# Optimization experiments

Measured on AMD Instinct MI355X. Metric: run time of the kernel, lower is better.

The kernel has to match this reference:

```python
import jax, jax.numpy as jnp
import numpy as np

N_NODES = 100000
N_FEAT = 500
N_HID = 16
N_CLS = 7
N_EDGES = 3200000


def setup_inputs() -> dict:
    key = jax.random.key(0)
    k1, k2, k3, k4 = jax.random.split(key, 4)
    x = jax.random.normal(k1, (N_NODES, N_FEAT), dtype=jnp.float32)
    edge_index = jax.random.randint(k2, (2, N_EDGES), 0, N_NODES, dtype=jnp.int32)
    # Glorot-style init for the two GCNConv weight matrices
    W1 = jax.random.normal(k3, (N_FEAT, N_HID), dtype=jnp.float32) * (1.0 / np.sqrt(N_FEAT))
    b1 = jnp.zeros((N_HID,), dtype=jnp.float32)
    W2 = jax.random.normal(k4, (N_HID, N_CLS), dtype=jnp.float32) * (1.0 / np.sqrt(N_HID))
    b2 = jnp.zeros((N_CLS,), dtype=jnp.float32)
    return {"x": x, "edge_index": edge_index, "W1": W1, "b1": b1, "W2": W2, "b2": b2}


def _gcn_norm(edge_index, n_nodes):
    # Add self-loops, compute symmetric normalization D^-1/2 (A+I) D^-1/2
    loop = jnp.arange(n_nodes, dtype=edge_index.dtype)
    src = jnp.concatenate([edge_index[0], loop])  # [E+N]
    dst = jnp.concatenate([edge_index[1], loop])  # [E+N]
    deg = jax.ops.segment_sum(jnp.ones_like(dst, dtype=jnp.float32), dst, num_segments=n_nodes)
    dinv = jnp.where(deg > 0, jax.lax.rsqrt(deg), 0.0)
    norm = dinv[src] * dinv[dst]  # [E+N]
    return src, dst, norm


def _gcn_conv(h, W, b, src, dst, norm, n_nodes):
    m = h @ W                                   # [N, out] dense projection first (small out dim)
    agg = jax.ops.segment_sum(m[src] * norm[:, None], dst, num_segments=n_nodes)
    return agg + b


def reference(x, edge_index, W1, b1, W2, b2):
    n = x.shape[0]
    src, dst, norm = _gcn_norm(edge_index, n)
    h = jax.nn.relu(_gcn_conv(x, W1, b1, src, dst, norm, n))
    # dropout is identity in eval mode (training=False)
    logits = _gcn_conv(h, W2, b2, src, dst, norm, n)
    return jax.nn.log_softmax(logits, axis=1)
```

## Files before the change

### kernel.cpp

```cpp
#include <hip/hip_runtime.h>
#include <math.h>

#define N_NODES 100000
#define N_EDGES 3200000
#define N_FEAT  500
#define NF4     125
#define N_HID   16
#define N_CLS   7

#define BKT_SHIFT 7
#define BKT_SIZE  128
#define NBKT      782
#define NBLK_BIN  256
#define EDGES_PER_BLK 12500
#define COUNTS_LEN (NBKT * NBLK_BIN)
#define NBLK_SCANA (COUNTS_LEN / 256)
#define SBUF_CAP  5632

#define OFF_DINV   0
#define OFF_COUNTS 100000
#define OFF_BSUM   300192
#define OFF_ROWP   301216
#define OFF_BINNED 401220
#define OFF_SORTED 3601220
#define OFF_M1S    6801220
#define OFF_M2S    7601220

typedef __attribute__((ext_vector_type(8))) short short8v;
typedef __attribute__((ext_vector_type(4))) float f32x4v;

__device__ inline unsigned short f2bf(float f) {
    unsigned int u = __float_as_uint(f);
    return (unsigned short)((u + 0x7FFF + ((u >> 16) & 1)) >> 16);
}
__device__ inline float bf2f(unsigned short h) {
    return __uint_as_float((unsigned int)h << 16);
}

__device__ inline void gload16(const void* g, void* l) {
    __builtin_amdgcn_global_load_lds(
        (const __attribute__((address_space(1))) void*)g,
        (__attribute__((address_space(3))) void*)l, 16, 0, 0);
}

__global__ void hist(const int* __restrict__ dst, int* __restrict__ counts) {
    __shared__ int cnt[NBKT];
    int t = threadIdx.x, b = blockIdx.x;
    for (int i = t; i < NBKT; i += 256) cnt[i] = 0;
    __syncthreads();
    int e0 = b * EDGES_PER_BLK;
    for (int e = e0 + t; e < e0 + EDGES_PER_BLK; e += 256)
        atomicAdd(&cnt[dst[e] >> BKT_SHIFT], 1);
    __syncthreads();
    for (int i = t; i < NBKT; i += 256)
        counts[i * NBLK_BIN + b] = cnt[i];
}

__global__ void scanA(int* __restrict__ counts, int* __restrict__ bsum) {
    __shared__ int s[256];
    int t = threadIdx.x;
    int i = blockIdx.x * 256 + t;
    int v = counts[i];
    s[t] = v;
    __syncthreads();
    for (int off = 1; off < 256; off <<= 1) {
        int a = (t >= off) ? s[t - off] : 0;
        __syncthreads();
        s[t] += a;
        __syncthreads();
    }
    counts[i] = s[t] - v;
    if (t == 255) bsum[blockIdx.x] = s[255];
}

__global__ void scanB(int* __restrict__ bsum) {
    __shared__ int s[1024];
    int t = threadIdx.x;
    int v = (t < NBLK_SCANA) ? bsum[t] : 0;
    s[t] = v;
    __syncthreads();
    for (int off = 1; off < 1024; off <<= 1) {
        int a = (t >= off) ? s[t - off] : 0;
        __syncthreads();
        s[t] += a;
        __syncthreads();
    }
    if (t < NBLK_SCANA) bsum[t] = s[t] - v;
}


__global__ void binpass(const int* __restrict__ src, const int* __restrict__ dst,
                        const int* __restrict__ counts, const int* __restrict__ bsum,
                        unsigned int* __restrict__ binned) {
    __shared__ int cur[NBKT];
    int t = threadIdx.x, b = blockIdx.x;
    for (int i = t; i < NBKT; i += 256) cur[i] = counts[i * NBLK_BIN + b] + bsum[i];
    __syncthreads();
    int e0 = b * EDGES_PER_BLK;
    for (int e = e0 + t; e < e0 + EDGES_PER_BLK; e += 256) {
        int d = dst[e];
        int pos = atomicAdd(&cur[d >> BKT_SHIFT], 1);
        binned[pos] = (unsigned int)src[e] | ((unsigned int)(d & (BKT_SIZE - 1)) << 17);
    }
}

__global__ __launch_bounds__(512) void sortpass(const unsigned int* __restrict__ binned,
        const int* __restrict__ counts, const int* __restrict__ bsum,
        unsigned int* __restrict__ sorted,
        int* __restrict__ rowptr, float* __restrict__ dinv) {
    __shared__ int cnt[BKT_SIZE];
    __shared__ int sc[BKT_SIZE];
    __shared__ int cur[BKT_SIZE];
    __shared__ unsigned int sbuf[SBUF_CAP];
    int t = threadIdx.x, b = blockIdx.x;
    int beg = counts[b * NBLK_BIN] + bsum[b];
    int end = (b < NBKT - 1) ? counts[(b + 1) * NBLK_BIN] + bsum[b + 1] : N_EDGES;
    if (t < BKT_SIZE) cnt[t] = 0;
    __syncthreads();
    for (int e = beg + t; e < end; e += 512)
        atomicAdd(&cnt[(binned[e] >> 17) & (BKT_SIZE - 1)], 1);
    __syncthreads();
    int v = (t < BKT_SIZE) ? cnt[t] : 0;
    if (t < BKT_SIZE) sc[t] = v;
    __syncthreads();
    for (int off = 1; off < BKT_SIZE; off <<= 1) {
        int a = (t < BKT_SIZE && t >= off) ? sc[t - off] : 0;
        __syncthreads();
        if (t < BKT_SIZE) sc[t] += a;
        __syncthreads();
    }
    if (t < BKT_SIZE) {
        cur[t] = sc[t] - v;
        int g = b * BKT_SIZE + t;
        if (g < N_NODES) {
            rowptr[g] = beg + sc[t] - v;
            dinv[g] = rsqrtf((float)v + 1.0f);
        }
    }
    if (b == 0 && t == 0) rowptr[N_NODES] = N_EDGES;
    __syncthreads();
    for (int e = beg + t; e < end; e += 512) {
        unsigned int u = binned[e];
        int pos = atomicAdd(&cur[(u >> 17) & (BKT_SIZE - 1)], 1);
        if (pos < SBUF_CAP) sbuf[pos] = u & 0x1FFFF;
    }
    __syncthreads();
    int n = end - beg;
    for (int i = t; i < n; i += 512) sorted[beg + i] = sbuf[i];
}

__global__ void wpack(const float* __restrict__ W1, uint4* __restrict__ wp) {
    int p = blockIdx.x * 256 + threadIdx.x;
    if (p >= 1024) return;
    int s = p >> 6, l = p & 63;
    int col = l & 15, kb = s * 32 + (l >> 4) * 8;
    unsigned int hw[4], lw[4];
#pragma unroll
    for (int d = 0; d < 4; ++d) {
        unsigned int hpair = 0, lpair = 0;
#pragma unroll
        for (int e = 0; e < 2; ++e) {
            int k = kb + d * 2 + e;
            float w0 = (k < N_FEAT) ? W1[k * 16 + col] : 0.f;
            unsigned int u = __float_as_uint(w0);
            unsigned int uh = u & 0xFFFF0000u;
            float res = w0 - __uint_as_float(uh);
            hpair |= (uh >> 16) << (16 * e);
            lpair |= (unsigned int)f2bf(res) << (16 * e);
        }
        hw[d] = hpair; lw[d] = lpair;
    }
    wp[p] = make_uint4(hw[0], hw[1], hw[2], hw[3]);
    wp[1024 + p] = make_uint4(lw[0], lw[1], lw[2], lw[3]);
}

#define G1_NBLK 1563

__device__ inline void split8(const float4 a, const float4 b, short8v& hi, short8v& lo) {
    float f[8] = {a.x, a.y, a.z, a.w, b.x, b.y, b.z, b.w};
#pragma unroll
    for (int i = 0; i < 8; ++i) {
        unsigned int u = __float_as_uint(f[i]);
        unsigned int uh = u & 0xFFFF0000u;
        hi[i] = (short)(u >> 16);
        lo[i] = (short)f2bf(f[i] - __uint_as_float(uh));
    }
}

__global__ __launch_bounds__(256) void gemm1(const float* __restrict__ x,
        const uint4* __restrict__ wp, const float* __restrict__ dinv,
        unsigned short* __restrict__ m1s) {
    __shared__ float lds[2][2048];
    const int t = threadIdx.x, b = blockIdx.x;
    const int lane = t & 63, w = t >> 6;
    const int rowbase = b * 64;
    const char* xb = (const char*)x;

    size_t gbase[2], gtail[2];
#pragma unroll
    for (int j = 0; j < 2; ++j) {
        int i = j * 256 + t;
        int row = i >> 3;
        int u = i & 7;
        int inner = (u * 16) ^ ((row & 7) << 4);
        int grow = rowbase + row; if (grow >= N_NODES) grow = 0;
        gbase[j] = (size_t)grow * 2000 + (size_t)inner;
        int tf = 480 + (inner >> 2);
        gtail[j] = (tf < 500) ? gbase[j] + 1920 : (size_t)0;
    }

    const int r16 = lane & 15, g = lane >> 4;
    const int lrow = w * 16 + r16;
    const int sw = (lrow & 7) << 4;
    const int off1 = lrow * 128 + ((g * 32) ^ sw);
    const int off2 = lrow * 128 + ((g * 32 + 16) ^ sw);

    f32x4v acc = {0.f, 0.f, 0.f, 0.f};

    gload16(xb + gbase[0], (void*)&lds[0][w * 256]);
    gload16(xb + gbase[1], (void*)&lds[0][1024 + w * 256]);
    __syncthreads();

    int cur = 0;
    for (int s = 0; s < 16; ++s) {
        if (s < 15) {
            int sn = s + 1;
            size_t a0 = (sn < 15) ? gbase[0] + (size_t)sn * 128 : gtail[0];
            size_t a1 = (sn < 15) ? gbase[1] + (size_t)sn * 128 : gtail[1];
            gload16(xb + a0, (void*)&lds[cur ^ 1][w * 256]);
            gload16(xb + a1, (void*)&lds[cur ^ 1][1024 + w * 256]);
        }
        short8v bh = *reinterpret_cast<const short8v*>(&wp[s * 64 + lane]);
        short8v bl = *reinterpret_cast<const short8v*>(&wp[1024 + s * 64 + lane]);
        const char* lb = (const char*)&lds[cur][0];
        float4 fa = *(const float4*)(lb + off1);
        float4 fb = *(const float4*)(lb + off2);
        short8v ah, al;
        split8(fa, fb, ah, al);
        acc = __builtin_amdgcn_mfma_f32_16x16x32_bf16(ah, bh, acc, 0, 0, 0);
        acc = __builtin_amdgcn_mfma_f32_16x16x32_bf16(al, bh, acc, 0, 0, 0);
        acc = __builtin_amdgcn_mfma_f32_16x16x32_bf16(ah, bl, acc, 0, 0, 0);
        __syncthreads();
        cur ^= 1;
    }

#pragma unroll
    for (int j = 0; j < 4; ++j) {
        int r = rowbase + w * 16 + g * 4 + j;
        if (r < N_NODES) m1s[(size_t)r * 16 + r16] = f2bf(acc[j] * dinv[r]);
    }
}

__global__ __launch_bounds__(512) void agg1(const unsigned int* __restrict__ sorted,
        const int* __restrict__ rowptr, const float* __restrict__ dinv,
        const unsigned short* __restrict__ m1s, const float* __restrict__ b1,
        const float* __restrict__ W2, unsigned short* __restrict__ m2s) {
    __shared__ float acc[BKT_SIZE * 17];
    __shared__ float sW2[N_HID * N_CLS];
    __shared__ float sb1[N_HID];
    int t = threadIdx.x, b = blockIdx.x;
    if (t < N_HID * N_CLS) sW2[t] = W2[t];
    if (t < N_HID) sb1[t] = b1[t];
    int n = t >> 2, q = t & 3;
    int g = b * BKT_SIZE + n;
    float a0 = 0.f, a1 = 0.f, a2 = 0.f, a3 = 0.f;
    if (g < N_NODES) {
        int beg = rowptr[g], end = rowptr[g + 1];
        int p = beg;
        for (; p + 1 < end; p += 2) {
            unsigned int s0 = sorted[p], s1 = sorted[p + 1];
            uint2 w0 = *(const uint2*)&m1s[(size_t)s0 * 16 + q * 4];
            uint2 w1 = *(const uint2*)&m1s[(size_t)s1 * 16 + q * 4];
            a0 += __uint_as_float(w0.x << 16);
            a1 += __uint_as_float(w0.x & 0xFFFF0000u);
            a2 += __uint_as_float(w0.y << 16);
            a3 += __uint_as_float(w0.y & 0xFFFF0000u);
            a0 += __uint_as_float(w1.x << 16);
            a1 += __uint_as_float(w1.x & 0xFFFF0000u);
            a2 += __uint_as_float(w1.y << 16);
            a3 += __uint_as_float(w1.y & 0xFFFF0000u);
        }
        if (p < end) {
            unsigned int s0 = sorted[p];
            uint2 w0 = *(const uint2*)&m1s[(size_t)s0 * 16 + q * 4];
            a0 += __uint_as_float(w0.x << 16);
            a1 += __uint_as_float(w0.x & 0xFFFF0000u);
            a2 += __uint_as_float(w0.y << 16);
            a3 += __uint_as_float(w0.y & 0xFFFF0000u);
        }
    }
    float* ap = &acc[n * 17 + q * 4];
    ap[0] = a0; ap[1] = a1; ap[2] = a2; ap[3] = a3;
    __syncthreads();
    for (int idx = t; idx < BKT_SIZE * 16; idx += 512) {
        int nn = idx >> 4, jj = idx & 15;
        int gg = b * BKT_SIZE + nn;
        if (gg < N_NODES) {
            float di = dinv[gg];
            float hv = di * (acc[nn * 17 + jj] + bf2f(m1s[(size_t)gg * 16 + jj])) + sb1[jj];
            acc[nn * 17 + jj] = hv > 0.f ? hv : 0.f;
        }
    }
    __syncthreads();
    for (int idx = t; idx < BKT_SIZE * 8; idx += 512) {
        int nn = idx >> 3, cc = idx & 7;
        int gg = b * BKT_SIZE + nn;
        if (gg < N_NODES) {
            float sum = 0.f;
            if (cc < N_CLS) {
#pragma unroll
                for (int jj = 0; jj < N_HID; ++jj) sum += acc[nn * 17 + jj] * sW2[jj * 7 + cc];
                sum *= dinv[gg];
            }
            m2s[(size_t)gg * 8 + cc] = f2bf(sum);
        }
    }
}

__global__ __launch_bounds__(256) void agg2(const unsigned int* __restrict__ sorted,
        const int* __restrict__ rowptr, const float* __restrict__ dinv,
        const unsigned short* __restrict__ m2s, const float* __restrict__ b2,
        float* __restrict__ out) {
    __shared__ float acc[BKT_SIZE * 9];
    int t = threadIdx.x, b = blockIdx.x;
    int n = t >> 1, q = t & 1;
    int g = b * BKT_SIZE + n;
    float a0 = 0.f, a1 = 0.f, a2 = 0.f, a3 = 0.f;
    if (g < N_NODES) {
        int beg = rowptr[g], end = rowptr[g + 1];
        int p = beg;
        for (; p + 1 < end; p += 2) {
            unsigned int s0 = sorted[p], s1 = sorted[p + 1];
            uint2 w0 = *(const uint2*)&m2s[(size_t)s0 * 8 + q * 4];
            uint2 w1 = *(const uint2*)&m2s[(size_t)s1 * 8 + q * 4];
            a0 += __uint_as_float(w0.x << 16);
            a1 += __uint_as_float(w0.x & 0xFFFF0000u);
            a2 += __uint_as_float(w0.y << 16);
            a3 += __uint_as_float(w0.y & 0xFFFF0000u);
            a0 += __uint_as_float(w1.x << 16);
            a1 += __uint_as_float(w1.x & 0xFFFF0000u);
            a2 += __uint_as_float(w1.y << 16);
            a3 += __uint_as_float(w1.y & 0xFFFF0000u);
        }
        if (p < end) {
            unsigned int s0 = sorted[p];
            uint2 w0 = *(const uint2*)&m2s[(size_t)s0 * 8 + q * 4];
            a0 += __uint_as_float(w0.x << 16);
            a1 += __uint_as_float(w0.x & 0xFFFF0000u);
            a2 += __uint_as_float(w0.y << 16);
            a3 += __uint_as_float(w0.y & 0xFFFF0000u);
        }
    }
    float* ap = &acc[n * 9 + q * 4];
    ap[0] = a0; ap[1] = a1; ap[2] = a2; ap[3] = a3;
    __syncthreads();
    int j = t & 7;
    for (int pass = 0; pass < 4; ++pass) {
        int nn = (t >> 3) + pass * 32;
        int gg = b * BKT_SIZE + nn;
        bool valid = (gg < N_NODES) && (j < N_CLS);
        float v = -1e30f;
        if (valid) {
            float di = dinv[gg];
            v = di * (acc[nn * 9 + j] + bf2f(m2s[(size_t)gg * 8 + j])) + b2[j];
        }
        float mx = v;
#pragma unroll
        for (int off = 1; off < 8; off <<= 1) mx = fmaxf(mx, __shfl_xor(mx, off, 8));
        float ex = valid ? expf(v - mx) : 0.f;
        float sum = ex;
#pragma unroll
        for (int off = 1; off < 8; off <<= 1) sum += __shfl_xor(sum, off, 8);
        float ls = mx + logf(sum);
        if (valid) out[(size_t)gg * 7 + j] = v - ls;
    }
}

extern "C" void kernel_launch(void* const* d_in, const int* in_sizes, int n_in,
                              void* d_out, int out_size, void* d_ws, size_t ws_size,
                              hipStream_t stream) {
    const float* x  = (const float*)d_in[0];
    const int*   ei = (const int*)d_in[1];
    const float* W1 = (const float*)d_in[2];
    const float* b1 = (const float*)d_in[3];
    const float* W2 = (const float*)d_in[4];
    const float* b2 = (const float*)d_in[5];
    float* out = (float*)d_out;
    char*  wsb = (char*)d_ws;

    const int* src = ei;
    const int* dst = ei + N_EDGES;

    float*          dinv   = (float*)wsb + OFF_DINV;
    int*            counts = (int*)wsb + OFF_COUNTS;
    int*            bsum   = (int*)wsb + OFF_BSUM;
    int*            rowptr = (int*)wsb + OFF_ROWP;
    unsigned int*   binned = (unsigned int*)wsb + OFF_BINNED;
    unsigned int*   sorted = (unsigned int*)wsb + OFF_SORTED;
    unsigned short* m1s    = (unsigned short*)(wsb + (size_t)OFF_M1S * 4);
    unsigned short* m2s    = (unsigned short*)(wsb + (size_t)OFF_M2S * 4);
    uint4*          wp     = (uint4*)binned;

    hist     <<<NBLK_BIN, 256, 0, stream>>>(dst, counts);
    scanA    <<<NBLK_SCANA, 256, 0, stream>>>(counts, bsum);
    scanB    <<<1, 1024, 0, stream>>>(bsum);
    binpass  <<<NBLK_BIN, 256, 0, stream>>>(src, dst, counts, bsum, binned);
    sortpass <<<NBKT, 512, 0, stream>>>(binned, counts, bsum, sorted, rowptr, dinv);
    wpack    <<<4, 256, 0, stream>>>(W1, wp);
    gemm1    <<<G1_NBLK, 256, 0, stream>>>(x, wp, dinv, m1s);
    agg1     <<<NBKT, 512, 0, stream>>>(sorted, rowptr, dinv, m1s, b1, W2, m2s);
    agg2     <<<NBKT, 256, 0, stream>>>(sorted, rowptr, dinv, m2s, b2, out);
}
```

Measured before the change: 497.3 us.

## Drop per-node CSR sort; aggregate bucketed edges with LDS float atomics

Removes the sortpass kernel that built per-node CSR order and rowptr. Degrees now come from global atomics in the histogram pass, with a small kernel computing dinv. The aggregation kernels walk each 128-node bucket's binned edges directly and accumulate into shared-memory rows with float atomicAdd, using staggered column order to spread bank conflicts. This saves the sort pass and its traffic, but adds many LDS atomics per edge, global atomics on deg, and a memset, and makes the summation order nondeterministic.

```diff
diff --git a/kernel.cpp b/kernel.cpp
--- a/kernel.cpp
+++ b/kernel.cpp
@@ -15,14 +15,13 @@
 #define EDGES_PER_BLK 12500
 #define COUNTS_LEN (NBKT * NBLK_BIN)
 #define NBLK_SCANA (COUNTS_LEN / 256)
-#define SBUF_CAP  5632
 
 #define OFF_DINV   0
 #define OFF_COUNTS 100000
 #define OFF_BSUM   300192
-#define OFF_ROWP   301216
+#define OFF_DEG    301216
 #define OFF_BINNED 401220
-#define OFF_SORTED 3601220
+#define OFF_WP     3601220
 #define OFF_M1S    6801220
 #define OFF_M2S    7601220
 
@@ -43,17 +42,26 @@
         (__attribute__((address_space(3))) void*)l, 16, 0, 0);
 }
 
-__global__ void hist(const int* __restrict__ dst, int* __restrict__ counts) {
+__global__ void hist(const int* __restrict__ dst, int* __restrict__ counts,
+                     int* __restrict__ deg) {
     __shared__ int cnt[NBKT];
     int t = threadIdx.x, b = blockIdx.x;
     for (int i = t; i < NBKT; i += 256) cnt[i] = 0;
     __syncthreads();
     int e0 = b * EDGES_PER_BLK;
-    for (int e = e0 + t; e < e0 + EDGES_PER_BLK; e += 256)
-        atomicAdd(&cnt[dst[e] >> BKT_SHIFT], 1);
+    for (int e = e0 + t; e < e0 + EDGES_PER_BLK; e += 256) {
+        int d = dst[e];
+        atomicAdd(&cnt[d >> BKT_SHIFT], 1);
+        atomicAdd(&deg[d], 1);
+    }
     __syncthreads();
     for (int i = t; i < NBKT; i += 256)
         counts[i * NBLK_BIN + b] = cnt[i];
+}
+
+__global__ void dinvK(const int* __restrict__ deg, float* __restrict__ dinv) {
+    int g = blockIdx.x * 256 + threadIdx.x;
+    if (g < N_NODES) dinv[g] = rsqrtf((float)deg[g] + 1.0f);
 }
 
 __global__ void scanA(int* __restrict__ counts, int* __restrict__ bsum) {
@@ -88,7 +96,6 @@
     if (t < NBLK_SCANA) bsum[t] = s[t] - v;
 }
 
-
 __global__ void binpass(const int* __restrict__ src, const int* __restrict__ dst,
                         const int* __restrict__ counts, const int* __restrict__ bsum,
                         unsigned int* __restrict__ binned) {
@@ -102,51 +109,6 @@
         int pos = atomicAdd(&cur[d >> BKT_SHIFT], 1);
         binned[pos] = (unsigned int)src[e] | ((unsigned int)(d & (BKT_SIZE - 1)) << 17);
     }
-}
-
-__global__ __launch_bounds__(512) void sortpass(const unsigned int* __restrict__ binned,
-        const int* __restrict__ counts, const int* __restrict__ bsum,
-        unsigned int* __restrict__ sorted,
-        int* __restrict__ rowptr, float* __restrict__ dinv) {
-    __shared__ int cnt[BKT_SIZE];
-    __shared__ int sc[BKT_SIZE];
-    __shared__ int cur[BKT_SIZE];
-    __shared__ unsigned int sbuf[SBUF_CAP];
-    int t = threadIdx.x, b = blockIdx.x;
-    int beg = counts[b * NBLK_BIN] + bsum[b];
-    int end = (b < NBKT - 1) ? counts[(b + 1) * NBLK_BIN] + bsum[b + 1] : N_EDGES;
-    if (t < BKT_SIZE) cnt[t] = 0;
-    __syncthreads();
-    for (int e = beg + t; e < end; e += 512)
-        atomicAdd(&cnt[(binned[e] >> 17) & (BKT_SIZE - 1)], 1);
-    __syncthreads();
-    int v = (t < BKT_SIZE) ? cnt[t] : 0;
-    if (t < BKT_SIZE) sc[t] = v;
-    __syncthreads();
-    for (int off = 1; off < BKT_SIZE; off <<= 1) {
-        int a = (t < BKT_SIZE && t >= off) ? sc[t - off] : 0;
-        __syncthreads();
-        if (t < BKT_SIZE) sc[t] += a;
-        __syncthreads();
-    }
-    if (t < BKT_SIZE) {
-        cur[t] = sc[t] - v;
-        int g = b * BKT_SIZE + t;
-        if (g < N_NODES) {
-            rowptr[g] = beg + sc[t] - v;
-            dinv[g] = rsqrtf((float)v + 1.0f);
-        }
-    }
-    if (b == 0 && t == 0) rowptr[N_NODES] = N_EDGES;
-    __syncthreads();
-    for (int e = beg + t; e < end; e += 512) {
-        unsigned int u = binned[e];
-        int pos = atomicAdd(&cur[(u >> 17) & (BKT_SIZE - 1)], 1);
-        if (pos < SBUF_CAP) sbuf[pos] = u & 0x1FFFF;
-    }
-    __syncthreads();
-    int n = end - beg;
-    for (int i = t; i < n; i += 512) sorted[beg + i] = sbuf[i];
 }
 
 __global__ void wpack(const float* __restrict__ W1, uint4* __restrict__ wp) {
@@ -251,48 +213,47 @@
     }
 }
 
-__global__ __launch_bounds__(512) void agg1(const unsigned int* __restrict__ sorted,
-        const int* __restrict__ rowptr, const float* __restrict__ dinv,
-        const unsigned short* __restrict__ m1s, const float* __restrict__ b1,
-        const float* __restrict__ W2, unsigned short* __restrict__ m2s) {
+__global__ __launch_bounds__(256) void bagg1(const unsigned int* __restrict__ binned,
+        const int* __restrict__ counts, const int* __restrict__ bsum,
+        const float* __restrict__ dinv, const unsigned short* __restrict__ m1s,
+        const float* __restrict__ b1, const float* __restrict__ W2,
+        unsigned short* __restrict__ m2s) {
     __shared__ float acc[BKT_SIZE * 17];
     __shared__ float sW2[N_HID * N_CLS];
     __shared__ float sb1[N_HID];
     int t = threadIdx.x, b = blockIdx.x;
     if (t < N_HID * N_CLS) sW2[t] = W2[t];
     if (t < N_HID) sb1[t] = b1[t];
-    int n = t >> 2, q = t & 3;
-    int g = b * BKT_SIZE + n;
-    float a0 = 0.f, a1 = 0.f, a2 = 0.f, a3 = 0.f;
-    if (g < N_NODES) {
-        int beg = rowptr[g], end = rowptr[g + 1];
-        int p = beg;
-        for (; p + 1 < end; p += 2) {
-            unsigned int s0 = sorted[p], s1 = sorted[p + 1];
-            uint2 w0 = *(const uint2*)&m1s[(size_t)s0 * 16 + q * 4];
-            uint2 w1 = *(const uint2*)&m1s[(size_t)s1 * 16 + q * 4];
-            a0 += __uint_as_float(w0.x << 16);
-            a1 += __uint_as_float(w0.x & 0xFFFF0000u);
-            a2 += __uint_as_float(w0.y << 16);
-            a3 += __uint_as_float(w0.y & 0xFFFF0000u);
-            a0 += __uint_as_float(w1.x << 16);
-            a1 += __uint_as_float(w1.x & 0xFFFF0000u);
-            a2 += __uint_as_float(w1.y << 16);
-            a3 += __uint_as_float(w1.y & 0xFFFF0000u);
-        }
-        if (p < end) {
-            unsigned int s0 = sorted[p];
-            uint2 w0 = *(const uint2*)&m1s[(size_t)s0 * 16 + q * 4];
-            a0 += __uint_as_float(w0.x << 16);
-            a1 += __uint_as_float(w0.x & 0xFFFF0000u);
-            a2 += __uint_as_float(w0.y << 16);
-            a3 += __uint_as_float(w0.y & 0xFFFF0000u);
-        }
-    }
-    float* ap = &acc[n * 17 + q * 4];
-    ap[0] = a0; ap[1] = a1; ap[2] = a2; ap[3] = a3;
-    __syncthreads();
-    for (int idx = t; idx < BKT_SIZE * 16; idx += 512) {
+    for (int i = t; i < BKT_SIZE * 17; i += 256) acc[i] = 0.f;
+    int beg = counts[b * NBLK_BIN] + bsum[b];
+    int end = (b < NBKT - 1) ? counts[(b + 1) * NBLK_BIN] + bsum[b + 1] : N_EDGES;
+    __syncthreads();
+    const int st = t & 15;
+    for (int e = beg + t; e < end; e += 256) {
+        unsigned int u = binned[e];
+        int s = u & 0x1FFFF;
+        float* ap = &acc[((u >> 17) & (BKT_SIZE - 1)) * 17];
+        uint4 w0 = *(const uint4*)&m1s[(size_t)s * 16];
+        uint4 w1 = *(const uint4*)&m1s[(size_t)s * 16 + 8];
+        float f[16];
+        f[0]  = __uint_as_float(w0.x << 16); f[1]  = __uint_as_float(w0.x & 0xFFFF0000u);
+        f[2]  = __uint_as_float(w0.y << 16); f[3]  = __uint_as_float(w0.y & 0xFFFF0000u);
+        f[4]  = __uint_as_float(w0.z << 16); f[5]  = __uint_as_float(w0.z & 0xFFFF0000u);
+        f[6]  = __uint_as_float(w0.w << 16); f[7]  = __uint_as_float(w0.w & 0xFFFF0000u);
+        f[8]  = __uint_as_float(w1.x << 16); f[9]  = __uint_as_float(w1.x & 0xFFFF0000u);
+        f[10] = __uint_as_float(w1.y << 16); f[11] = __uint_as_float(w1.y & 0xFFFF0000u);
+        f[12] = __uint_as_float(w1.z << 16); f[13] = __uint_as_float(w1.w == 0 ? 0.f : __float_as_uint(0.f));
+        f[13] = __uint_as_float(w1.z & 0xFFFF0000u);
+        f[14] = __uint_as_float(w1.w << 16); f[15] = __uint_as_float(w1.w & 0xFFFF0000u);
+        f[12] = __uint_as_float(w1.z << 16);
+#pragma unroll
+        for (int i = 0; i < 16; ++i) {
+            int j = (i + st) & 15;
+            atomicAdd(&ap[j], f[j]);
+        }
+    }
+    __syncthreads();
+    for (int idx = t; idx < BKT_SIZE * 16; idx += 256) {
         int nn = idx >> 4, jj = idx & 15;
         int gg = b * BKT_SIZE + nn;
         if (gg < N_NODES) {
@@ -302,7 +263,7 @@
         }
     }
     __syncthreads();
-    for (int idx = t; idx < BKT_SIZE * 8; idx += 512) {
+    for (int idx = t; idx < BKT_SIZE * 8; idx += 256) {
         int nn = idx >> 3, cc = idx & 7;
         int gg = b * BKT_SIZE + nn;
         if (gg < N_NODES) {
@@ -317,42 +278,33 @@
     }
 }
 
-__global__ __launch_bounds__(256) void agg2(const unsigned int* __restrict__ sorted,
-        const int* __restrict__ rowptr, const float* __restrict__ dinv,
-        const unsigned short* __restrict__ m2s, const float* __restrict__ b2,
-        float* __restrict__ out) {
+__global__ __launch_bounds__(256) void bagg2(const unsigned int* __restrict__ binned,
+        const int* __restrict__ counts, const int* __restrict__ bsum,
+        const float* __restrict__ dinv, const unsigned short* __restrict__ m2s,
+        const float* __restrict__ b2, float* __restrict__ out) {
     __shared__ float acc[BKT_SIZE * 9];
     int t = threadIdx.x, b = blockIdx.x;
-    int n = t >> 1, q = t & 1;
-    int g = b * BKT_SIZE + n;
-    float a0 = 0.f, a1 = 0.f, a2 = 0.f, a3 = 0.f;
-    if (g < N_NODES) {
-        int beg = rowptr[g], end = rowptr[g + 1];
-        int p = beg;
-        for (; p + 1 < end; p += 2) {
-            unsigned int s0 = sorted[p], s1 = sorted[p + 1];
-            uint2 w0 = *(const uint2*)&m2s[(size_t)s0 * 8 + q * 4];
-            uint2 w1 = *(const uint2*)&m2s[(size_t)s1 * 8 + q * 4];
-            a0 += __uint_as_float(w0.x << 16);
-            a1 += __uint_as_float(w0.x & 0xFFFF0000u);
-            a2 += __uint_as_float(w0.y << 16);
-            a3 += __uint_as_float(w0.y & 0xFFFF0000u);
-            a0 += __uint_as_float(w1.x << 16);
-            a1 += __uint_as_float(w1.x & 0xFFFF0000u);
-            a2 += __uint_as_float(w1.y << 16);
-            a3 += __uint_as_float(w1.y & 0xFFFF0000u);
-        }
-        if (p < end) {
-            unsigned int s0 = sorted[p];
-            uint2 w0 = *(const uint2*)&m2s[(size_t)s0 * 8 + q * 4];
-            a0 += __uint_as_float(w0.x << 16);
-            a1 += __uint_as_float(w0.x & 0xFFFF0000u);
-            a2 += __uint_as_float(w0.y << 16);
-            a3 += __uint_as_float(w0.y & 0xFFFF0000u);
-        }
-    }
-    float* ap = &acc[n * 9 + q * 4];
-    ap[0] = a0; ap[1] = a1; ap[2] = a2; ap[3] = a3;
+    for (int i = t; i < BKT_SIZE * 9; i += 256) acc[i] = 0.f;
+    int beg = counts[b * NBLK_BIN] + bsum[b];
+    int end = (b < NBKT - 1) ? counts[(b + 1) * NBLK_BIN] + bsum[b + 1] : N_EDGES;
+    __syncthreads();
+    const int st = t & 7;
+    for (int e = beg + t; e < end; e += 256) {
+        unsigned int u = binned[e];
+        int s = u & 0x1FFFF;
+        float* ap = &acc[((u >> 17) & (BKT_SIZE - 1)) * 9];
+        uint4 w0 = *(const uint4*)&m2s[(size_t)s * 8];
+        float f[8];
+        f[0] = __uint_as_float(w0.x << 16); f[1] = __uint_as_float(w0.x & 0xFFFF0000u);
+        f[2] = __uint_as_float(w0.y << 16); f[3] = __uint_as_float(w0.y & 0xFFFF0000u);
+        f[4] = __uint_as_float(w0.z << 16); f[5] = __uint_as_float(w0.z & 0xFFFF0000u);
+        f[6] = __uint_as_float(w0.w << 16); f[7] = __uint_as_float(w0.w & 0xFFFF0000u);
+#pragma unroll
+        for (int i = 0; i < 8; ++i) {
+            int j = (i + st) & 7;
+            atomicAdd(&ap[j], f[j]);
+        }
+    }
     __syncthreads();
     int j = t & 7;
     for (int pass = 0; pass < 4; ++pass) {
@@ -394,20 +346,20 @@
     float*          dinv   = (float*)wsb + OFF_DINV;
     int*            counts = (int*)wsb + OFF_COUNTS;
     int*            bsum   = (int*)wsb + OFF_BSUM;
-    int*            rowptr = (int*)wsb + OFF_ROWP;
+    int*            deg    = (int*)wsb + OFF_DEG;
     unsigned int*   binned = (unsigned int*)wsb + OFF_BINNED;
-    unsigned int*   sorted = (unsigned int*)wsb + OFF_SORTED;
+    uint4*          wp     = (uint4*)((int*)wsb + OFF_WP);
     unsigned short* m1s    = (unsigned short*)(wsb + (size_t)OFF_M1S * 4);
     unsigned short* m2s    = (unsigned short*)(wsb + (size_t)OFF_M2S * 4);
-    uint4*          wp     = (uint4*)binned;
-
-    hist     <<<NBLK_BIN, 256, 0, stream>>>(dst, counts);
-    scanA    <<<NBLK_SCANA, 256, 0, stream>>>(counts, bsum);
-    scanB    <<<1, 1024, 0, stream>>>(bsum);
-    binpass  <<<NBLK_BIN, 256, 0, stream>>>(src, dst, counts, bsum, binned);
-    sortpass <<<NBKT, 512, 0, stream>>>(binned, counts, bsum, sorted, rowptr, dinv);
-    wpack    <<<4, 256, 0, stream>>>(W1, wp);
-    gemm1    <<<G1_NBLK, 256, 0, stream>>>(x, wp, dinv, m1s);
-    agg1     <<<NBKT, 512, 0, stream>>>(sorted, rowptr, dinv, m1s, b1, W2, m2s);
-    agg2     <<<NBKT, 256, 0, stream>>>(sorted, rowptr, dinv, m2s, b2, out);
-}
+
+    hipMemsetAsync(deg, 0, N_NODES * sizeof(int), stream);
+    hist    <<<NBLK_BIN, 256, 0, stream>>>(dst, counts, deg);
+    dinvK   <<<391, 256, 0, stream>>>(deg, dinv);
+    scanA   <<<NBLK_SCANA, 256, 0, stream>>>(counts, bsum);
+    scanB   <<<1, 1024, 0, stream>>>(bsum);
+    binpass <<<NBLK_BIN, 256, 0, stream>>>(src, dst, counts, bsum, binned);
+    wpack   <<<4, 256, 0, stream>>>(W1, wp);
+    gemm1   <<<G1_NBLK, 256, 0, stream>>>(x, wp, dinv, m1s);
+    bagg1   <<<NBKT, 256, 0, stream>>>(binned, counts, bsum, dinv, m1s, b1, W2, m2s);
+    bagg2   <<<NBKT, 256, 0, stream>>>(binned, counts, bsum, dinv, m2s, b2, out);
+}
```

Result: slower. 1.029 ms (+107.0%).

## Replace two-level bucket sort CSR build with global-atomic degree count and scatter

Applied to the files above, without the earlier changes.

Replaces the histogram/bin/local-sort pipeline for building the destination-sorted CSR with a direct approach. Per-node degrees are counted with global atomics, prefix-scanned into row offsets, and edges are scattered with global atomicAdd on the row pointers. After the scatter, each row pointer holds its row's end offset, and the aggregation kernels read that shifted form. This removes one full pass over the edges and the binned intermediate buffer. In exchange it relies on 3.2M contended global atomics and random scattered writes, and the order of edges within a row becomes nondeterministic.

```diff
diff --git a/kernel.cpp b/kernel.cpp
--- a/kernel.cpp
+++ b/kernel.cpp
@@ -4,27 +4,21 @@
 #define N_NODES 100000
 #define N_EDGES 3200000
 #define N_FEAT  500
-#define NF4     125
 #define N_HID   16
 #define N_CLS   7
 
-#define BKT_SHIFT 7
 #define BKT_SIZE  128
 #define NBKT      782
-#define NBLK_BIN  256
-#define EDGES_PER_BLK 12500
-#define COUNTS_LEN (NBKT * NBLK_BIN)
-#define NBLK_SCANA (COUNTS_LEN / 256)
-#define SBUF_CAP  5632
+#define NSCAN_BLK 392
 
 #define OFF_DINV   0
-#define OFF_COUNTS 100000
-#define OFF_BSUM   300192
-#define OFF_ROWP   301216
-#define OFF_BINNED 401220
-#define OFF_SORTED 3601220
-#define OFF_M1S    6801220
-#define OFF_M2S    7601220
+#define OFF_DEG    100000
+#define OFF_BSUM   200352
+#define OFF_ROWP   200864
+#define OFF_SORTED 300864
+#define OFF_WP     3500864
+#define OFF_M1S    3509056
+#define OFF_M2S    4309056
 
 typedef __attribute__((ext_vector_type(8))) short short8v;
 typedef __attribute__((ext_vector_type(4))) float f32x4v;
@@ -43,24 +37,17 @@
         (__attribute__((address_space(3))) void*)l, 16, 0, 0);
 }
 
-__global__ void hist(const int* __restrict__ dst, int* __restrict__ counts) {
-    __shared__ int cnt[NBKT];
-    int t = threadIdx.x, b = blockIdx.x;
-    for (int i = t; i < NBKT; i += 256) cnt[i] = 0;
-    __syncthreads();
-    int e0 = b * EDGES_PER_BLK;
-    for (int e = e0 + t; e < e0 + EDGES_PER_BLK; e += 256)
-        atomicAdd(&cnt[dst[e] >> BKT_SHIFT], 1);
-    __syncthreads();
-    for (int i = t; i < NBKT; i += 256)
-        counts[i * NBLK_BIN + b] = cnt[i];
-}
-
-__global__ void scanA(int* __restrict__ counts, int* __restrict__ bsum) {
+__global__ void degcnt(const int* __restrict__ dst, int* __restrict__ deg) {
+    int i = blockIdx.x * 256 + threadIdx.x;
+    for (int e = i; e < N_EDGES; e += 2048 * 256)
+        atomicAdd(&deg[dst[e]], 1);
+}
+
+__global__ void scanA(int* __restrict__ deg, int* __restrict__ bsum) {
     __shared__ int s[256];
     int t = threadIdx.x;
     int i = blockIdx.x * 256 + t;
-    int v = counts[i];
+    int v = deg[i];
     s[t] = v;
     __syncthreads();
     for (int off = 1; off < 256; off <<= 1) {
@@ -69,84 +56,43 @@
         s[t] += a;
         __syncthreads();
     }
-    counts[i] = s[t] - v;
+    deg[i] = s[t] - v;
     if (t == 255) bsum[blockIdx.x] = s[255];
 }
 
 __global__ void scanB(int* __restrict__ bsum) {
-    __shared__ int s[1024];
+    __shared__ int s[512];
     int t = threadIdx.x;
-    int v = (t < NBLK_SCANA) ? bsum[t] : 0;
+    int v = (t < NSCAN_BLK) ? bsum[t] : 0;
     s[t] = v;
     __syncthreads();
-    for (int off = 1; off < 1024; off <<= 1) {
+    for (int off = 1; off < 512; off <<= 1) {
         int a = (t >= off) ? s[t - off] : 0;
         __syncthreads();
         s[t] += a;
         __syncthreads();
     }
-    if (t < NBLK_SCANA) bsum[t] = s[t] - v;
-}
-
-
-__global__ void binpass(const int* __restrict__ src, const int* __restrict__ dst,
-                        const int* __restrict__ counts, const int* __restrict__ bsum,
-                        unsigned int* __restrict__ binned) {
-    __shared__ int cur[NBKT];
-    int t = threadIdx.x, b = blockIdx.x;
-    for (int i = t; i < NBKT; i += 256) cur[i] = counts[i * NBLK_BIN + b] + bsum[i];
-    __syncthreads();
-    int e0 = b * EDGES_PER_BLK;
-    for (int e = e0 + t; e < e0 + EDGES_PER_BLK; e += 256) {
-        int d = dst[e];
-        int pos = atomicAdd(&cur[d >> BKT_SHIFT], 1);
-        binned[pos] = (unsigned int)src[e] | ((unsigned int)(d & (BKT_SIZE - 1)) << 17);
-    }
-}
-
-__global__ __launch_bounds__(512) void sortpass(const unsigned int* __restrict__ binned,
-        const int* __restrict__ counts, const int* __restrict__ bsum,
-        unsigned int* __restrict__ sorted,
-        int* __restrict__ rowptr, float* __restrict__ dinv) {
-    __shared__ int cnt[BKT_SIZE];
-    __shared__ int sc[BKT_SIZE];
-    __shared__ int cur[BKT_SIZE];
-    __shared__ unsigned int sbuf[SBUF_CAP];
-    int t = threadIdx.x, b = blockIdx.x;
-    int beg = counts[b * NBLK_BIN] + bsum[b];
-    int end = (b < NBKT - 1) ? counts[(b + 1) * NBLK_BIN] + bsum[b + 1] : N_EDGES;
-    if (t < BKT_SIZE) cnt[t] = 0;
-    __syncthreads();
-    for (int e = beg + t; e < end; e += 512)
-        atomicAdd(&cnt[(binned[e] >> 17) & (BKT_SIZE - 1)], 1);
-    __syncthreads();
-    int v = (t < BKT_SIZE) ? cnt[t] : 0;
-    if (t < BKT_SIZE) sc[t] = v;
-    __syncthreads();
-    for (int off = 1; off < BKT_SIZE; off <<= 1) {
-        int a = (t < BKT_SIZE && t >= off) ? sc[t - off] : 0;
-        __syncthreads();
-        if (t < BKT_SIZE) sc[t] += a;
-        __syncthreads();
-    }
-    if (t < BKT_SIZE) {
-        cur[t] = sc[t] - v;
-        int g = b * BKT_SIZE + t;
-        if (g < N_NODES) {
-            rowptr[g] = beg + sc[t] - v;
-            dinv[g] = rsqrtf((float)v + 1.0f);
-        }
-    }
-    if (b == 0 && t == 0) rowptr[N_NODES] = N_EDGES;
-    __syncthreads();
-    for (int e = beg + t; e < end; e += 512) {
-        unsigned int u = binned[e];
-        int pos = atomicAdd(&cur[(u >> 17) & (BKT_SIZE - 1)], 1);
-        if (pos < SBUF_CAP) sbuf[pos] = u & 0x1FFFF;
-    }
-    __syncthreads();
-    int n = end - beg;
-    for (int i = t; i < n; i += 512) sorted[beg + i] = sbuf[i];
+    if (t < NSCAN_BLK) bsum[t] = s[t] - v;
+}
+
+__global__ void rowdinv(const int* __restrict__ deg, const int* __restrict__ bsum,
+                        int* __restrict__ rowp, float* __restrict__ dinv) {
+    int i = blockIdx.x * 256 + threadIdx.x;
+    if (i < N_NODES) {
+        int rp = deg[i] + bsum[i >> 8];
+        int nx = deg[i + 1] + bsum[(i + 1) >> 8];
+        rowp[i] = rp;
+        dinv[i] = rsqrtf((float)(nx - rp) + 1.0f);
+    }
+}
+
+__global__ void scatter(const int* __restrict__ src, const int* __restrict__ dst,
+                        int* __restrict__ rowp, unsigned int* __restrict__ sorted) {
+    int i = blockIdx.x * 256 + threadIdx.x;
+    for (int e = i; e < N_EDGES; e += 2048 * 256) {
+        int pos = atomicAdd(&rowp[dst[e]], 1);
+        sorted[pos] = (unsigned int)src[e];
+    }
 }
 
 __global__ void wpack(const float* __restrict__ W1, uint4* __restrict__ wp) {
@@ -252,7 +198,7 @@
 }
 
 __global__ __launch_bounds__(512) void agg1(const unsigned int* __restrict__ sorted,
-        const int* __restrict__ rowptr, const float* __restrict__ dinv,
+        const int* __restrict__ rowp, const float* __restrict__ dinv,
         const unsigned short* __restrict__ m1s, const float* __restrict__ b1,
         const float* __restrict__ W2, unsigned short* __restrict__ m2s) {
     __shared__ float acc[BKT_SIZE * 17];
@@ -265,7 +211,8 @@
     int g = b * BKT_SIZE + n;
     float a0 = 0.f, a1 = 0.f, a2 = 0.f, a3 = 0.f;
     if (g < N_NODES) {
-        int beg = rowptr[g], end = rowptr[g + 1];
+        int beg = g ? rowp[g - 1] : 0;
+        int end = rowp[g];
         int p = beg;
         for (; p + 1 < end; p += 2) {
             unsigned int s0 = sorted[p], s1 = sorted[p + 1];
@@ -318,7 +265,7 @@
 }
 
 __global__ __launch_bounds__(256) void agg2(const unsigned int* __restrict__ sorted,
-        const int* __restrict__ rowptr, const float* __restrict__ dinv,
+        const int* __restrict__ rowp, const float* __restrict__ dinv,
         const unsigned short* __restrict__ m2s, const float* __restrict__ b2,
         float* __restrict__ out) {
     __shared__ float acc[BKT_SIZE * 9];
@@ -327,7 +274,8 @@
     int g = b * BKT_SIZE + n;
     float a0 = 0.f, a1 = 0.f, a2 = 0.f, a3 = 0.f;
     if (g < N_NODES) {
-        int beg = rowptr[g], end = rowptr[g + 1];
+        int beg = g ? rowp[g - 1] : 0;
+        int end = rowp[g];
         int p = beg;
         for (; p + 1 < end; p += 2) {
             unsigned int s0 = sorted[p], s1 = sorted[p + 1];
@@ -392,22 +340,22 @@
     const int* dst = ei + N_EDGES;
 
     float*          dinv   = (float*)wsb + OFF_DINV;
-    int*            counts = (int*)wsb + OFF_COUNTS;
+    int*            deg    = (int*)wsb + OFF_DEG;
     int*            bsum   = (int*)wsb + OFF_BSUM;
-    int*            rowptr = (int*)wsb + OFF_ROWP;
-    unsigned int*   binned = (unsigned int*)wsb + OFF_BINNED;
+    int*            rowp   = (int*)wsb + OFF_ROWP;
     unsigned int*   sorted = (unsigned int*)wsb + OFF_SORTED;
+    uint4*          wp     = (uint4*)((int*)wsb + OFF_WP);
     unsigned short* m1s    = (unsigned short*)(wsb + (size_t)OFF_M1S * 4);
     unsigned short* m2s    = (unsigned short*)(wsb + (size_t)OFF_M2S * 4);
-    uint4*          wp     = (uint4*)binned;
-
-    hist     <<<NBLK_BIN, 256, 0, stream>>>(dst, counts);
-    scanA    <<<NBLK_SCANA, 256, 0, stream>>>(counts, bsum);
-    scanB    <<<1, 1024, 0, stream>>>(bsum);
-    binpass  <<<NBLK_BIN, 256, 0, stream>>>(src, dst, counts, bsum, binned);
-    sortpass <<<NBKT, 512, 0, stream>>>(binned, counts, bsum, sorted, rowptr, dinv);
-    wpack    <<<4, 256, 0, stream>>>(W1, wp);
-    gemm1    <<<G1_NBLK, 256, 0, stream>>>(x, wp, dinv, m1s);
-    agg1     <<<NBKT, 512, 0, stream>>>(sorted, rowptr, dinv, m1s, b1, W2, m2s);
-    agg2     <<<NBKT, 256, 0, stream>>>(sorted, rowptr, dinv, m2s, b2, out);
-}
+
+    hipMemsetAsync(deg, 0, (NSCAN_BLK * 256) * sizeof(int), stream);
+    degcnt  <<<2048, 256, 0, stream>>>(dst, deg);
+    scanA   <<<NSCAN_BLK, 256, 0, stream>>>(deg, bsum);
+    scanB   <<<1, 512, 0, stream>>>(bsum);
+    rowdinv <<<NSCAN_BLK, 256, 0, stream>>>(deg, bsum, rowp, dinv);
+    scatter <<<2048, 256, 0, stream>>>(src, dst, rowp, sorted);
+    wpack   <<<4, 256, 0, stream>>>(W1, wp);
+    gemm1   <<<G1_NBLK, 256, 0, stream>>>(x, wp, dinv, m1s);
+    agg1    <<<NBKT, 512, 0, stream>>>(sorted, rowp, dinv, m1s, b1, W2, m2s);
+    agg2    <<<NBKT, 256, 0, stream>>>(sorted, rowp, dinv, m2s, b2, out);
+}
```

New measurement: 797.7 us. +60.4%, slower.

## Split sort pass and fuse scatter-sort into first aggregation kernel

Applied to the files above, without the earlier changes.

The bucket sort is split so that the first pass only computes per-node counts, rowptr and dinv. The scatter into sorted order moves into the layer-1 aggregation kernel, which keeps the sorted source indices in LDS and gathers from there instead of re-reading them from global memory. The sorted array is still written out for agg2, and wp gets its own workspace slot because binned is now read after gemm1. This adds LDS pressure to the aggregation kernel, which may lower its occupancy.

```diff
diff --git a/kernel.cpp b/kernel.cpp
--- a/kernel.cpp
+++ b/kernel.cpp
@@ -23,8 +23,9 @@
 #define OFF_ROWP   301216
 #define OFF_BINNED 401220
 #define OFF_SORTED 3601220
-#define OFF_M1S    6801220
-#define OFF_M2S    7601220
+#define OFF_WP     6801220
+#define OFF_M1S    6809412
+#define OFF_M2S    7609412
 
 typedef __attribute__((ext_vector_type(8))) short short8v;
 typedef __attribute__((ext_vector_type(4))) float f32x4v;
@@ -88,7 +89,6 @@
     if (t < NBLK_SCANA) bsum[t] = s[t] - v;
 }
 
-
 __global__ void binpass(const int* __restrict__ src, const int* __restrict__ dst,
                         const int* __restrict__ counts, const int* __restrict__ bsum,
                         unsigned int* __restrict__ binned) {
@@ -104,14 +104,11 @@
     }
 }
 
-__global__ __launch_bounds__(512) void sortpass(const unsigned int* __restrict__ binned,
+__global__ __launch_bounds__(512) void sortA(const unsigned int* __restrict__ binned,
         const int* __restrict__ counts, const int* __restrict__ bsum,
-        unsigned int* __restrict__ sorted,
         int* __restrict__ rowptr, float* __restrict__ dinv) {
     __shared__ int cnt[BKT_SIZE];
     __shared__ int sc[BKT_SIZE];
-    __shared__ int cur[BKT_SIZE];
-    __shared__ unsigned int sbuf[SBUF_CAP];
     int t = threadIdx.x, b = blockIdx.x;
     int beg = counts[b * NBLK_BIN] + bsum[b];
     int end = (b < NBKT - 1) ? counts[(b + 1) * NBLK_BIN] + bsum[b + 1] : N_EDGES;
@@ -130,7 +127,6 @@
         __syncthreads();
     }
     if (t < BKT_SIZE) {
-        cur[t] = sc[t] - v;
         int g = b * BKT_SIZE + t;
         if (g < N_NODES) {
             rowptr[g] = beg + sc[t] - v;
@@ -138,15 +134,6 @@
         }
     }
     if (b == 0 && t == 0) rowptr[N_NODES] = N_EDGES;
-    __syncthreads();
-    for (int e = beg + t; e < end; e += 512) {
-        unsigned int u = binned[e];
-        int pos = atomicAdd(&cur[(u >> 17) & (BKT_SIZE - 1)], 1);
-        if (pos < SBUF_CAP) sbuf[pos] = u & 0x1FFFF;
-    }
-    __syncthreads();
-    int n = end - beg;
-    for (int i = t; i < n; i += 512) sorted[beg + i] = sbuf[i];
 }
 
 __global__ void wpack(const float* __restrict__ W1, uint4* __restrict__ wp) {
@@ -251,46 +238,69 @@
     }
 }
 
-__global__ __launch_bounds__(512) void agg1(const unsigned int* __restrict__ sorted,
+__global__ __launch_bounds__(512) void sortAgg1(const unsigned int* __restrict__ binned,
+        const int* __restrict__ counts, const int* __restrict__ bsum,
         const int* __restrict__ rowptr, const float* __restrict__ dinv,
         const unsigned short* __restrict__ m1s, const float* __restrict__ b1,
-        const float* __restrict__ W2, unsigned short* __restrict__ m2s) {
+        const float* __restrict__ W2, unsigned int* __restrict__ sorted,
+        unsigned short* __restrict__ m2s) {
+    __shared__ unsigned int sbuf[SBUF_CAP];
+    __shared__ int cur[BKT_SIZE];
     __shared__ float acc[BKT_SIZE * 17];
     __shared__ float sW2[N_HID * N_CLS];
     __shared__ float sb1[N_HID];
     int t = threadIdx.x, b = blockIdx.x;
     if (t < N_HID * N_CLS) sW2[t] = W2[t];
     if (t < N_HID) sb1[t] = b1[t];
-    int n = t >> 2, q = t & 3;
-    int g = b * BKT_SIZE + n;
-    float a0 = 0.f, a1 = 0.f, a2 = 0.f, a3 = 0.f;
-    if (g < N_NODES) {
-        int beg = rowptr[g], end = rowptr[g + 1];
-        int p = beg;
-        for (; p + 1 < end; p += 2) {
-            unsigned int s0 = sorted[p], s1 = sorted[p + 1];
-            uint2 w0 = *(const uint2*)&m1s[(size_t)s0 * 16 + q * 4];
-            uint2 w1 = *(const uint2*)&m1s[(size_t)s1 * 16 + q * 4];
-            a0 += __uint_as_float(w0.x << 16);
-            a1 += __uint_as_float(w0.x & 0xFFFF0000u);
-            a2 += __uint_as_float(w0.y << 16);
-            a3 += __uint_as_float(w0.y & 0xFFFF0000u);
-            a0 += __uint_as_float(w1.x << 16);
-            a1 += __uint_as_float(w1.x & 0xFFFF0000u);
-            a2 += __uint_as_float(w1.y << 16);
-            a3 += __uint_as_float(w1.y & 0xFFFF0000u);
-        }
-        if (p < end) {
-            unsigned int s0 = sorted[p];
-            uint2 w0 = *(const uint2*)&m1s[(size_t)s0 * 16 + q * 4];
-            a0 += __uint_as_float(w0.x << 16);
-            a1 += __uint_as_float(w0.x & 0xFFFF0000u);
-            a2 += __uint_as_float(w0.y << 16);
-            a3 += __uint_as_float(w0.y & 0xFFFF0000u);
-        }
-    }
-    float* ap = &acc[n * 17 + q * 4];
-    ap[0] = a0; ap[1] = a1; ap[2] = a2; ap[3] = a3;
+    int beg = counts[b * NBLK_BIN] + bsum[b];
+    int end = (b < NBKT - 1) ? counts[(b + 1) * NBLK_BIN] + bsum[b + 1] : N_EDGES;
+    if (t < BKT_SIZE) {
+        int g = b * BKT_SIZE + t;
+        cur[t] = ((g < N_NODES) ? rowptr[g] : end) - beg;
+    }
+    __syncthreads();
+    for (int e = beg + t; e < end; e += 512) {
+        unsigned int u = binned[e];
+        int pos = atomicAdd(&cur[(u >> 17) & (BKT_SIZE - 1)], 1);
+        if (pos < SBUF_CAP) sbuf[pos] = u & 0x1FFFF;
+    }
+    __syncthreads();
+    int n = end - beg;
+    for (int i = t; i < n; i += 512) sorted[beg + i] = sbuf[i];
+    {
+        int nn = t >> 2, q = t & 3;
+        int g = b * BKT_SIZE + nn;
+        float a0 = 0.f, a1 = 0.f, a2 = 0.f, a3 = 0.f;
+        if (g < N_NODES) {
+            int lbeg = rowptr[g] - beg;
+            int lend = ((g + 1 <= N_NODES) ? rowptr[g + 1] : N_EDGES) - beg;
+            int p = lbeg;
+            for (; p + 1 < lend; p += 2) {
+                unsigned int s0 = sbuf[p], s1 = sbuf[p + 1];
+                uint2 w0 = *(const uint2*)&m1s[(size_t)s0 * 16 + q * 4];
+                uint2 w1 = *(const uint2*)&m1s[(size_t)s1 * 16 + q * 4];
+                a0 += __uint_as_float(w0.x << 16);
+                a1 += __uint_as_float(w0.x & 0xFFFF0000u);
+                a2 += __uint_as_float(w0.y << 16);
+                a3 += __uint_as_float(w0.y & 0xFFFF0000u);
+                a0 += __uint_as_float(w1.x << 16);
+                a1 += __uint_as_float(w1.x & 0xFFFF0000u);
+                a2 += __uint_as_float(w1.y << 16);
+                a3 += __uint_as_float(w1.y & 0xFFFF0000u);
+            }
+            if (p < lend) {
+                unsigned int s0 = sbuf[p];
+                uint2 w0 = *(const uint2*)&m1s[(size_t)s0 * 16 + q * 4];
+                a0 += __uint_as_float(w0.x << 16);
+                a1 += __uint_as_float(w0.x & 0xFFFF0000u);
+                a2 += __uint_as_float(w0.y << 16);
+                a3 += __uint_as_float(w0.y & 0xFFFF0000u);
+            }
+        }
+        __syncthreads();
+        float* ap = &acc[nn * 17 + q * 4];
+        ap[0] = a0; ap[1] = a1; ap[2] = a2; ap[3] = a3;
+    }
     __syncthreads();
     for (int idx = t; idx < BKT_SIZE * 16; idx += 512) {
         int nn = idx >> 4, jj = idx & 15;
@@ -397,17 +407,18 @@
     int*            rowptr = (int*)wsb + OFF_ROWP;
     unsigned int*   binned = (unsigned int*)wsb + OFF_BINNED;
     unsigned int*   sorted = (unsigned int*)wsb + OFF_SORTED;
+    uint4*          wp     = (uint4*)((int*)wsb + OFF_WP);
     unsigned short* m1s    = (unsigned short*)(wsb + (size_t)OFF_M1S * 4);
     unsigned short* m2s    = (unsigned short*)(wsb + (size_t)OFF_M2S * 4);
-    uint4*          wp     = (uint4*)binned;
 
     hist     <<<NBLK_BIN, 256, 0, stream>>>(dst, counts);
     scanA    <<<NBLK_SCANA, 256, 0, stream>>>(counts, bsum);
     scanB    <<<1, 1024, 0, stream>>>(bsum);
     binpass  <<<NBLK_BIN, 256, 0, stream>>>(src, dst, counts, bsum, binned);
-    sortpass <<<NBKT, 512, 0, stream>>>(binned, counts, bsum, sorted, rowptr, dinv);
+    sortA    <<<NBKT, 512, 0, stream>>>(binned, counts, bsum, rowptr, dinv);
     wpack    <<<4, 256, 0, stream>>>(W1, wp);
     gemm1    <<<G1_NBLK, 256, 0, stream>>>(x, wp, dinv, m1s);
-    agg1     <<<NBKT, 512, 0, stream>>>(sorted, rowptr, dinv, m1s, b1, W2, m2s);
+    sortAgg1 <<<NBKT, 512, 0, stream>>>(binned, counts, bsum, rowptr, dinv,
+                                        m1s, b1, W2, sorted, m2s);
     agg2     <<<NBKT, 256, 0, stream>>>(sorted, rowptr, dinv, m2s, b2, out);
 }
```

Result: faster. 477.4 us (-4.0%).
